# Kernel optimization log

Hardware: AMD Instinct MI355X
Metric: run time of the kernel (lower is better)

## Reference

```python
import jax, jax.numpy as jnp
import numpy as np

N = 100000
E = 3200000
F_IN = 128
HID = 128
NC = 10
G = 512  # number of graphs in batch


def setup_inputs() -> dict:
    key = jax.random.key(0)
    ks = jax.random.split(key, 9)
    x = jax.random.normal(ks[0], (N, F_IN), dtype=jnp.float32)
    edge_index = jax.random.randint(ks[1], (2, E), 0, N, dtype=jnp.int64)
    batch = jnp.sort(jax.random.randint(ks[2], (N,), 0, G, dtype=jnp.int64))
    s = 1.0 / np.sqrt(F_IN)
    W1 = jax.random.uniform(ks[3], (F_IN, HID), jnp.float32, -s, s)
    b1 = jnp.zeros((HID,), jnp.float32)
    sh = 1.0 / np.sqrt(HID)
    W2 = jax.random.uniform(ks[4], (HID, HID), jnp.float32, -sh, sh)
    b2 = jnp.zeros((HID,), jnp.float32)
    Wc = jax.random.uniform(ks[5], (HID, NC), jnp.float32, -sh, sh)
    bc = jax.random.uniform(ks[6], (NC,), jnp.float32, -sh, sh)
    return {"x": x, "edge_index": edge_index, "batch": batch,
            "W1": W1, "b1": b1, "W2": W2, "b2": b2, "Wc": Wc, "bc": bc}


def _gcn_conv(x, src, dst, norm, W, b):
    # linear transform first (PyG GCNConv), then normalized scatter-add
    h = x @ W                              # [N, H]
    msg = h[src] * norm[:, None]           # gather + scale, [E+N, H]
    out = jax.ops.segment_sum(msg, dst, num_segments=N)
    return out + b


def reference(x, edge_index, batch, W1, b1, W2, b2, Wc, bc):
    # add self-loops (PyG gcn_norm default)
    loop = jnp.arange(N, dtype=edge_index.dtype)
    src = jnp.concatenate([edge_index[0], loop])
    dst = jnp.concatenate([edge_index[1], loop])
    deg = jax.ops.segment_sum(jnp.ones_like(dst, dtype=x.dtype), dst, num_segments=N)
    dis = jnp.where(deg > 0, jax.lax.rsqrt(deg), 0.0)  # deg^{-1/2}
    norm = dis[src] * dis[dst]

    h = jax.nn.relu(_gcn_conv(x, src, dst, norm, W1, b1))
    # dropout is identity in eval mode
    h = jax.nn.relu(_gcn_conv(h, src, dst, norm, W2, b2))

    # global mean pool over graph ids
    sums = jax.ops.segment_sum(h, batch, num_segments=G)
    cnts = jax.ops.segment_sum(jnp.ones((N,), h.dtype), batch, num_segments=G)
    pooled = sums / jnp.maximum(cnts, 1.0)[:, None]   # [G, HID]

    logits = pooled @ Wc + bc                          # [G, NC]
    return logits, pooled
```

## Files before the change

kernel.cpp:

```cpp
#include <hip/hip_runtime.h>
#include <hip/hip_bf16.h>

typedef short bf16x8 __attribute__((ext_vector_type(8)));
typedef float f32x4 __attribute__((ext_vector_type(4)));
typedef unsigned int u32x4 __attribute__((ext_vector_type(4)));

__device__ __forceinline__ unsigned short f2bf(float f) {
    unsigned int u = __float_as_uint(f);
    unsigned int r = u + 0x7fffu + ((u >> 16) & 1u);
    return (unsigned short)(r >> 16);
}
__device__ __forceinline__ float bf2f(unsigned short b) {
    return __uint_as_float(((unsigned int)b) << 16);
}

__global__ __launch_bounds__(256) void cast_bf_k(const float* __restrict__ x, unsigned short* __restrict__ o, int n4) {
    int i = blockIdx.x * 256 + threadIdx.x;
    if (i < n4) {
        float4 v = ((const float4*)x)[i];
        ushort4 r;
        r.x = f2bf(v.x); r.y = f2bf(v.y); r.z = f2bf(v.z); r.w = f2bf(v.w);
        ((ushort4*)o)[i] = r;
    }
}

__global__ __launch_bounds__(256) void hist_k(const int* __restrict__ dst, int* __restrict__ hist,
                                              int e, int nbuk, int nblk, int eb) {
    __shared__ int lh[512];
    int blk = blockIdx.x, t = threadIdx.x;
    for (int j = t; j < nbuk; j += 256) lh[j] = 0;
    __syncthreads();
    int e0 = blk * eb, e1 = min(e, e0 + eb);
    for (int i = e0 + t; i < e1; i += 256) atomicAdd(&lh[dst[i] >> 8], 1);
    __syncthreads();
    for (int j = t; j < nbuk; j += 256) hist[(size_t)j * nblk + blk] = lh[j];
}

__global__ __launch_bounds__(256) void scanA_k(int* __restrict__ hist, int* __restrict__ btot, int nbuk, int nblk) {
    int w = (blockIdx.x * 256 + threadIdx.x) >> 6;
    int lane = threadIdx.x & 63;
    if (w >= nbuk) return;
    size_t base = (size_t)w * nblk;
    int run = 0;
    for (int c = 0; c < nblk; c += 64) {
        int i = c + lane;
        int v = (i < nblk) ? hist[base + i] : 0;
        int orig = v;
        for (int d = 1; d < 64; d <<= 1) { int u = __shfl_up(v, d); if (lane >= d) v += u; }
        if (i < nblk) hist[base + i] = run + v - orig;
        run += __shfl(v, 63);
    }
    if (lane == 0) btot[w] = run;
}

__global__ __launch_bounds__(512) void scanB_k(const int* __restrict__ btot, int* __restrict__ bbase, int nbuk) {
    __shared__ int s[512];
    int t = threadIdx.x;
    int v = (t < nbuk) ? btot[t] : 0;
    s[t] = v;
    __syncthreads();
    for (int st = 1; st < 512; st <<= 1) {
        int add = (t >= st) ? s[t - st] : 0;
        __syncthreads();
        s[t] += add;
        __syncthreads();
    }
    if (t < nbuk) bbase[t] = s[t] - v;
    if (t == nbuk - 1) bbase[nbuk] = s[t];
}

__global__ __launch_bounds__(256) void scatter_k(const int* __restrict__ src, const int* __restrict__ dst,
                                                 const int* __restrict__ hist, const int* __restrict__ bbase,
                                                 unsigned int* __restrict__ coarse, int e, int nbuk, int nblk, int eb) {
    __shared__ int cur[512];
    int blk = blockIdx.x, t = threadIdx.x;
    for (int j = t; j < nbuk; j += 256) cur[j] = bbase[j] + hist[(size_t)j * nblk + blk];
    __syncthreads();
    int e0 = blk * eb, e1 = min(e, e0 + eb);
    for (int i = e0 + t; i < e1; i += 256) {
        int s = src[i], d = dst[i];
        int bk = d >> 8;
        int p = atomicAdd(&cur[bk], 1);
        coarse[p] = ((unsigned int)(d & 255) << 24) | (unsigned int)s;
    }
}

__global__ __launch_bounds__(256) void bucket_k(const unsigned int* __restrict__ coarse, const int* __restrict__ bbase,
                                                int* __restrict__ cnt, int* __restrict__ row_ptr, int* __restrict__ col,
                                                int n, int nbuk, int e) {
    __shared__ int h[256];
    __shared__ int s[256];
    __shared__ int cur[256];
    int b = blockIdx.x, t = threadIdx.x;
    int e0 = bbase[b], e1 = bbase[b + 1];
    h[t] = 0;
    __syncthreads();
    for (int i = e0 + t; i < e1; i += 256) atomicAdd(&h[coarse[i] >> 24], 1);
    __syncthreads();
    int v = h[t];
    s[t] = v;
    __syncthreads();
    for (int st = 1; st < 256; st <<= 1) {
        int add = (t >= st) ? s[t - st] : 0;
        __syncthreads();
        s[t] += add;
        __syncthreads();
    }
    int excl = s[t] - v;
    int node = b * 256 + t;
    if (node < n) { cnt[node] = v; row_ptr[node] = e0 + excl; }
    cur[t] = e0 + excl;
    __syncthreads();
    for (int i = e0 + t; i < e1; i += 256) {
        unsigned int pk = coarse[i];
        int p = atomicAdd(&cur[pk >> 24], 1);
        col[p] = (int)(pk & 0x00FFFFFFu);
    }
    if (b == nbuk - 1 && t == 0) row_ptr[n] = e;
}

__global__ __launch_bounds__(256) void dis_k(const int* __restrict__ cnt, float* __restrict__ dis, int n) {
    int i = blockIdx.x * 256 + threadIdx.x;
    if (i < n) dis[i] = rsqrtf((float)cnt[i] + 1.0f);
}

__global__ __launch_bounds__(256) void gemm_mfma_k(const unsigned short* __restrict__ A, const float* __restrict__ W,
                                                   const float* __restrict__ dis, unsigned short* __restrict__ C,
                                                   int nrows) {
    __shared__ unsigned short WT[128 * 136];
    int t = threadIdx.x;
    for (int i = t; i < 16384; i += 256) {
        int k = i >> 7, nn = i & 127;
        WT[nn * 136 + k] = f2bf(W[i]);
    }
    __syncthreads();
    int wave = t >> 6, lane = t & 63;
    int lm = lane & 15, lg = lane >> 4;
    for (int m0 = blockIdx.x * 64; m0 < nrows; m0 += gridDim.x * 64) {
        int R = m0 + wave * 16;
        int arow = R + lm;
        if (arow >= nrows) arow = nrows - 1;
        const u32x4* ap = (const u32x4*)(A + (size_t)arow * 128);
        f32x4 acc[8];
#pragma unroll
        for (int q = 0; q < 8; q++) acc[q] = (f32x4){0.f, 0.f, 0.f, 0.f};
#pragma unroll
        for (int kk = 0; kk < 4; kk++) {
            bf16x8 af = __builtin_bit_cast(bf16x8, ap[kk * 4 + lg]);
#pragma unroll
            for (int q = 0; q < 8; q++) {
                const u32x4* bp = (const u32x4*)(WT + (q * 16 + lm) * 136 + kk * 32 + lg * 8);
                bf16x8 bfr = __builtin_bit_cast(bf16x8, *bp);
                acc[q] = __builtin_amdgcn_mfma_f32_16x16x32_bf16(af, bfr, acc[q], 0, 0, 0);
            }
        }
        float dsc[4];
#pragma unroll
        for (int i2 = 0; i2 < 4; i2++) {
            int r = R + lg * 4 + i2;
            dsc[i2] = (r < nrows) ? dis[r] : 0.f;
        }
#pragma unroll
        for (int i2 = 0; i2 < 4; i2++) {
            int r = R + lg * 4 + i2;
            if (r < nrows) {
                unsigned short* cp = C + (size_t)r * 128 + lm;
#pragma unroll
                for (int q = 0; q < 8; q++) cp[q * 16] = f2bf(acc[q][i2] * dsc[i2]);
            }
        }
    }
}

__global__ __launch_bounds__(256) void agg_k(const unsigned short* __restrict__ h, unsigned short* __restrict__ out,
                                             const int* __restrict__ row_ptr, const int* __restrict__ col,
                                             const float* __restrict__ dis, const float* __restrict__ bias, int n) {
    int wid  = (blockIdx.x * 256 + threadIdx.x) >> 6;
    int lane = threadIdx.x & 63;
    if (wid >= n) return;
    const unsigned int* hp = (const unsigned int*)h;
    unsigned int hv = hp[(size_t)wid * 64 + lane];
    float accx = __uint_as_float(hv << 16);
    float accy = __uint_as_float(hv & 0xffff0000u);
    int e = row_ptr[wid], e1 = row_ptr[wid + 1];
    for (; e + 8 <= e1; e += 8) {
        int c0 = col[e],     c1 = col[e + 1], c2 = col[e + 2], c3 = col[e + 3];
        int c4 = col[e + 4], c5 = col[e + 5], c6 = col[e + 6], c7 = col[e + 7];
        unsigned int h0 = hp[(size_t)c0 * 64 + lane];
        unsigned int h1 = hp[(size_t)c1 * 64 + lane];
        unsigned int h2 = hp[(size_t)c2 * 64 + lane];
        unsigned int h3 = hp[(size_t)c3 * 64 + lane];
        unsigned int h4 = hp[(size_t)c4 * 64 + lane];
        unsigned int h5 = hp[(size_t)c5 * 64 + lane];
        unsigned int h6 = hp[(size_t)c6 * 64 + lane];
        unsigned int h7 = hp[(size_t)c7 * 64 + lane];
        accx += __uint_as_float(h0 << 16) + __uint_as_float(h1 << 16)
              + __uint_as_float(h2 << 16) + __uint_as_float(h3 << 16)
              + __uint_as_float(h4 << 16) + __uint_as_float(h5 << 16)
              + __uint_as_float(h6 << 16) + __uint_as_float(h7 << 16);
        accy += __uint_as_float(h0 & 0xffff0000u) + __uint_as_float(h1 & 0xffff0000u)
              + __uint_as_float(h2 & 0xffff0000u) + __uint_as_float(h3 & 0xffff0000u)
              + __uint_as_float(h4 & 0xffff0000u) + __uint_as_float(h5 & 0xffff0000u)
              + __uint_as_float(h6 & 0xffff0000u) + __uint_as_float(h7 & 0xffff0000u);
    }
    for (; e < e1; e++) {
        unsigned int hh = hp[(size_t)col[e] * 64 + lane];
        accx += __uint_as_float(hh << 16);
        accy += __uint_as_float(hh & 0xffff0000u);
    }
    float d = dis[wid];
    float2 b = ((const float2*)bias)[lane];
    unsigned int res = ((unsigned int)f2bf(fmaxf(b.y + d * accy, 0.f)) << 16)
                     |  (unsigned int)f2bf(fmaxf(b.x + d * accx, 0.f));
    ((unsigned int*)out)[(size_t)wid * 64 + lane] = res;
}

__global__ __launch_bounds__(128) void pool_k(const unsigned short* __restrict__ h, const int* __restrict__ batch,
                                              float* __restrict__ pooled, int n) {
    int g = blockIdx.x;
    int j = threadIdx.x;
    int lo = 0, hi = n;
    while (lo < hi) { int mid = (lo + hi) >> 1; if (batch[mid] < g) lo = mid + 1; else hi = mid; }
    int start = lo;
    hi = n;
    while (lo < hi) { int mid = (lo + hi) >> 1; if (batch[mid] < g + 1) lo = mid + 1; else hi = mid; }
    int end = lo;
    float acc = 0.f;
    for (int r = start; r < end; r++) acc += bf2f(h[(size_t)r * 128 + j]);
    float cntf = (float)(end - start);
    pooled[(size_t)g * 128 + j] = acc / fmaxf(cntf, 1.0f);
}

__global__ __launch_bounds__(64) void logits_k(const float* __restrict__ pooled, const float* __restrict__ Wc,
                                               const float* __restrict__ bc, float* __restrict__ out, int nc) {
    int g = blockIdx.x;
    int j = threadIdx.x;
    if (j >= nc) return;
    float acc = bc[j];
    const float* p = pooled + (size_t)g * 128;
#pragma unroll 8
    for (int k = 0; k < 128; k++) acc += p[k] * Wc[k * nc + j];
    out[(size_t)g * nc + j] = acc;
}

extern "C" void kernel_launch(void* const* d_in, const int* in_sizes, int n_in,
                              void* d_out, int out_size, void* d_ws, size_t ws_size,
                              hipStream_t stream) {
    const float* x     = (const float*)d_in[0];
    const int*   ei    = (const int*)d_in[1];
    const int*   batch = (const int*)d_in[2];
    const float* W1    = (const float*)d_in[3];
    const float* b1    = (const float*)d_in[4];
    const float* W2    = (const float*)d_in[5];
    const float* b2    = (const float*)d_in[6];
    const float* Wc    = (const float*)d_in[7];
    const float* bc    = (const float*)d_in[8];
    float* out = (float*)d_out;

    const int N = in_sizes[0] / 128;
    const int E = in_sizes[1] / 2;
    const int NC = 10;
    const int G = out_size / (NC + 128);

    const int* src = ei;
    const int* dst = ei + E;

    const int EB   = 16384;
    const int NBLK = (E + EB - 1) / EB;
    const int NBUK = (N + 255) / 256;

    char* wbase = (char*)d_ws;
    size_t off = 0;
    auto alloc = [&](size_t bytes) -> void* {
        void* p = wbase + off;
        off = (off + bytes + 255) & ~(size_t)255;
        return p;
    };
    int*   cnt     = (int*)alloc((size_t)N * 4);
    float* dis     = (float*)alloc((size_t)N * 4);
    int*   row_ptr = (int*)alloc((size_t)(N + 1) * 4);
    int*   hist    = (int*)alloc((size_t)NBUK * NBLK * 4);
    int*   btot    = (int*)alloc((size_t)NBUK * 4);
    int*   bbase   = (int*)alloc((size_t)(NBUK + 1) * 4);
    unsigned int* coarse = (unsigned int*)alloc((size_t)E * 4);
    int*   col     = (int*)alloc((size_t)E * 4);
    unsigned short* bufX = (unsigned short*)alloc((size_t)N * 128 * 2);
    unsigned short* bufT = (unsigned short*)alloc((size_t)N * 128 * 2);
    unsigned short* bufH = (unsigned short*)alloc((size_t)N * 128 * 2);

    hist_k<<<NBLK, 256, 0, stream>>>(dst, hist, E, NBUK, NBLK, EB);
    scanA_k<<<(NBUK * 64 + 255) / 256, 256, 0, stream>>>(hist, btot, NBUK, NBLK);
    scanB_k<<<1, 512, 0, stream>>>(btot, bbase, NBUK);
    scatter_k<<<NBLK, 256, 0, stream>>>(src, dst, hist, bbase, coarse, E, NBUK, NBLK, EB);
    bucket_k<<<NBUK, 256, 0, stream>>>(coarse, bbase, cnt, row_ptr, col, N, NBUK, E);
    dis_k<<<(N + 255) / 256, 256, 0, stream>>>(cnt, dis, N);

    cast_bf_k<<<(N * 128 / 4 + 255) / 256, 256, 0, stream>>>(x, bufX, N * 128 / 4);

    gemm_mfma_k<<<512, 256, 0, stream>>>(bufX, W1, dis, bufT, N);
    agg_k<<<(N + 3) / 4, 256, 0, stream>>>(bufT, bufH, row_ptr, col, dis, b1, N);
    gemm_mfma_k<<<512, 256, 0, stream>>>(bufH, W2, dis, bufT, N);
    agg_k<<<(N + 3) / 4, 256, 0, stream>>>(bufT, bufH, row_ptr, col, dis, b2, N);

    float* pooled = out + (size_t)G * NC;
    pool_k<<<G, 128, 0, stream>>>(bufH, batch, pooled, N);
    logits_k<<<G, 64, 0, stream>>>(pooled, Wc, bc, out, NC);
}
```

Measured before the change: 431.8 us.

## Vectorize aggregation gathers with 16-byte loads and fuse small kernels

The aggregation kernel now splits each wavefront into four groups of 16 lanes. Each lane loads 16 bytes per neighbor row, and each group handles every fourth edge. Partial sums are combined with cross-lane shuffles before the bias, ReLU and bf16 store. Separately, the degree-normalization kernel is folded into bucket_k, and pooling and logits are fused into one kernel, which removes launches and an intermediate count buffer. The wider loads should cut the number of memory instructions per gathered row and raise bytes in flight, at the cost of extra shuffle reductions and idle lanes on low-degree nodes.

```diff
diff --git a/kernel.cpp b/kernel.cpp
--- a/kernel.cpp
+++ b/kernel.cpp
@@ -12,6 +12,9 @@
 }
 __device__ __forceinline__ float bf2f(unsigned short b) {
     return __uint_as_float(((unsigned int)b) << 16);
+}
+__device__ __forceinline__ unsigned int packbf2(float lo, float hi) {
+    return ((unsigned int)f2bf(hi) << 16) | (unsigned int)f2bf(lo);
 }
 
 __global__ __launch_bounds__(256) void cast_bf_k(const float* __restrict__ x, unsigned short* __restrict__ o, int n4) {
@@ -86,7 +89,7 @@
 }
 
 __global__ __launch_bounds__(256) void bucket_k(const unsigned int* __restrict__ coarse, const int* __restrict__ bbase,
-                                                int* __restrict__ cnt, int* __restrict__ row_ptr, int* __restrict__ col,
+                                                float* __restrict__ dis, int* __restrict__ row_ptr, int* __restrict__ col,
                                                 int n, int nbuk, int e) {
     __shared__ int h[256];
     __shared__ int s[256];
@@ -108,7 +111,10 @@
     }
     int excl = s[t] - v;
     int node = b * 256 + t;
-    if (node < n) { cnt[node] = v; row_ptr[node] = e0 + excl; }
+    if (node < n) {
+        row_ptr[node] = e0 + excl;
+        dis[node] = rsqrtf((float)v + 1.0f);
+    }
     cur[t] = e0 + excl;
     __syncthreads();
     for (int i = e0 + t; i < e1; i += 256) {
@@ -117,11 +123,6 @@
         col[p] = (int)(pk & 0x00FFFFFFu);
     }
     if (b == nbuk - 1 && t == 0) row_ptr[n] = e;
-}
-
-__global__ __launch_bounds__(256) void dis_k(const int* __restrict__ cnt, float* __restrict__ dis, int n) {
-    int i = blockIdx.x * 256 + threadIdx.x;
-    if (i < n) dis[i] = rsqrtf((float)cnt[i] + 1.0f);
 }
 
 __global__ __launch_bounds__(256) void gemm_mfma_k(const unsigned short* __restrict__ A, const float* __restrict__ W,
@@ -178,45 +179,56 @@
     int wid  = (blockIdx.x * 256 + threadIdx.x) >> 6;
     int lane = threadIdx.x & 63;
     if (wid >= n) return;
-    const unsigned int* hp = (const unsigned int*)h;
-    unsigned int hv = hp[(size_t)wid * 64 + lane];
-    float accx = __uint_as_float(hv << 16);
-    float accy = __uint_as_float(hv & 0xffff0000u);
-    int e = row_ptr[wid], e1 = row_ptr[wid + 1];
-    for (; e + 8 <= e1; e += 8) {
-        int c0 = col[e],     c1 = col[e + 1], c2 = col[e + 2], c3 = col[e + 3];
-        int c4 = col[e + 4], c5 = col[e + 5], c6 = col[e + 6], c7 = col[e + 7];
-        unsigned int h0 = hp[(size_t)c0 * 64 + lane];
-        unsigned int h1 = hp[(size_t)c1 * 64 + lane];
-        unsigned int h2 = hp[(size_t)c2 * 64 + lane];
-        unsigned int h3 = hp[(size_t)c3 * 64 + lane];
-        unsigned int h4 = hp[(size_t)c4 * 64 + lane];
-        unsigned int h5 = hp[(size_t)c5 * 64 + lane];
-        unsigned int h6 = hp[(size_t)c6 * 64 + lane];
-        unsigned int h7 = hp[(size_t)c7 * 64 + lane];
-        accx += __uint_as_float(h0 << 16) + __uint_as_float(h1 << 16)
-              + __uint_as_float(h2 << 16) + __uint_as_float(h3 << 16)
-              + __uint_as_float(h4 << 16) + __uint_as_float(h5 << 16)
-              + __uint_as_float(h6 << 16) + __uint_as_float(h7 << 16);
-        accy += __uint_as_float(h0 & 0xffff0000u) + __uint_as_float(h1 & 0xffff0000u)
-              + __uint_as_float(h2 & 0xffff0000u) + __uint_as_float(h3 & 0xffff0000u)
-              + __uint_as_float(h4 & 0xffff0000u) + __uint_as_float(h5 & 0xffff0000u)
-              + __uint_as_float(h6 & 0xffff0000u) + __uint_as_float(h7 & 0xffff0000u);
-    }
-    for (; e < e1; e++) {
-        unsigned int hh = hp[(size_t)col[e] * 64 + lane];
-        accx += __uint_as_float(hh << 16);
-        accy += __uint_as_float(hh & 0xffff0000u);
-    }
-    float d = dis[wid];
-    float2 b = ((const float2*)bias)[lane];
-    unsigned int res = ((unsigned int)f2bf(fmaxf(b.y + d * accy, 0.f)) << 16)
-                     |  (unsigned int)f2bf(fmaxf(b.x + d * accx, 0.f));
-    ((unsigned int*)out)[(size_t)wid * 64 + lane] = res;
-}
-
-__global__ __launch_bounds__(128) void pool_k(const unsigned short* __restrict__ h, const int* __restrict__ batch,
-                                              float* __restrict__ pooled, int n) {
+    int g = lane >> 4;
+    int s = lane & 15;
+    const char* hb = (const char*)h;
+    unsigned int soff = (unsigned int)(s << 4);
+    float acc0 = 0.f, acc1 = 0.f, acc2 = 0.f, acc3 = 0.f;
+    float acc4 = 0.f, acc5 = 0.f, acc6 = 0.f, acc7 = 0.f;
+#define ACCUM(v)                                                                              \
+    acc0 += __uint_as_float((v)[0] << 16); acc1 += __uint_as_float((v)[0] & 0xffff0000u);     \
+    acc2 += __uint_as_float((v)[1] << 16); acc3 += __uint_as_float((v)[1] & 0xffff0000u);     \
+    acc4 += __uint_as_float((v)[2] << 16); acc5 += __uint_as_float((v)[2] & 0xffff0000u);     \
+    acc6 += __uint_as_float((v)[3] << 16); acc7 += __uint_as_float((v)[3] & 0xffff0000u);
+    if (g == 0) {
+        u32x4 v = *(const u32x4*)(hb + (((unsigned int)wid << 8) + soff));
+        ACCUM(v)
+    }
+    int e = row_ptr[wid] + g, e1 = row_ptr[wid + 1];
+    for (; e + 4 < e1; e += 8) {
+        unsigned int o0 = ((unsigned int)col[e] << 8) + soff;
+        unsigned int o1 = ((unsigned int)col[e + 4] << 8) + soff;
+        u32x4 v0 = *(const u32x4*)(hb + o0);
+        u32x4 v1 = *(const u32x4*)(hb + o1);
+        ACCUM(v0)
+        ACCUM(v1)
+    }
+    if (e < e1) {
+        u32x4 v0 = *(const u32x4*)(hb + (((unsigned int)col[e] << 8) + soff));
+        ACCUM(v0)
+    }
+#undef ACCUM
+#define RED(a) a += __shfl_xor(a, 16); a += __shfl_xor(a, 32);
+    RED(acc0) RED(acc1) RED(acc2) RED(acc3) RED(acc4) RED(acc5) RED(acc6) RED(acc7)
+#undef RED
+    if (g == 0) {
+        float d = dis[wid];
+        const float4* bp = (const float4*)bias;
+        float4 ba = bp[2 * s], bb = bp[2 * s + 1];
+        u32x4 r;
+        r[0] = packbf2(fmaxf(ba.x + d * acc0, 0.f), fmaxf(ba.y + d * acc1, 0.f));
+        r[1] = packbf2(fmaxf(ba.z + d * acc2, 0.f), fmaxf(ba.w + d * acc3, 0.f));
+        r[2] = packbf2(fmaxf(bb.x + d * acc4, 0.f), fmaxf(bb.y + d * acc5, 0.f));
+        r[3] = packbf2(fmaxf(bb.z + d * acc6, 0.f), fmaxf(bb.w + d * acc7, 0.f));
+        *(u32x4*)((char*)out + (((unsigned int)wid << 8) + soff)) = r;
+    }
+}
+
+__global__ __launch_bounds__(128) void pool_logits_k(const unsigned short* __restrict__ h, const int* __restrict__ batch,
+                                                     const float* __restrict__ Wc, const float* __restrict__ bc,
+                                                     float* __restrict__ logits, float* __restrict__ pooled,
+                                                     int n, int nc) {
+    __shared__ float pl[128];
     int g = blockIdx.x;
     int j = threadIdx.x;
     int lo = 0, hi = n;
@@ -227,20 +239,16 @@
     int end = lo;
     float acc = 0.f;
     for (int r = start; r < end; r++) acc += bf2f(h[(size_t)r * 128 + j]);
-    float cntf = (float)(end - start);
-    pooled[(size_t)g * 128 + j] = acc / fmaxf(cntf, 1.0f);
-}
-
-__global__ __launch_bounds__(64) void logits_k(const float* __restrict__ pooled, const float* __restrict__ Wc,
-                                               const float* __restrict__ bc, float* __restrict__ out, int nc) {
-    int g = blockIdx.x;
-    int j = threadIdx.x;
-    if (j >= nc) return;
-    float acc = bc[j];
-    const float* p = pooled + (size_t)g * 128;
+    float pv = acc / fmaxf((float)(end - start), 1.0f);
+    pooled[(size_t)g * 128 + j] = pv;
+    pl[j] = pv;
+    __syncthreads();
+    if (j < nc) {
+        float a = bc[j];
 #pragma unroll 8
-    for (int k = 0; k < 128; k++) acc += p[k] * Wc[k * nc + j];
-    out[(size_t)g * nc + j] = acc;
+        for (int k = 0; k < 128; k++) a += pl[k] * Wc[k * nc + j];
+        logits[(size_t)g * nc + j] = a;
+    }
 }
 
 extern "C" void kernel_launch(void* const* d_in, const int* in_sizes, int n_in,
@@ -276,7 +284,6 @@
         off = (off + bytes + 255) & ~(size_t)255;
         return p;
     };
-    int*   cnt     = (int*)alloc((size_t)N * 4);
     float* dis     = (float*)alloc((size_t)N * 4);
     int*   row_ptr = (int*)alloc((size_t)(N + 1) * 4);
     int*   hist    = (int*)alloc((size_t)NBUK * NBLK * 4);
@@ -292,8 +299,7 @@
     scanA_k<<<(NBUK * 64 + 255) / 256, 256, 0, stream>>>(hist, btot, NBUK, NBLK);
     scanB_k<<<1, 512, 0, stream>>>(btot, bbase, NBUK);
     scatter_k<<<NBLK, 256, 0, stream>>>(src, dst, hist, bbase, coarse, E, NBUK, NBLK, EB);
-    bucket_k<<<NBUK, 256, 0, stream>>>(coarse, bbase, cnt, row_ptr, col, N, NBUK, E);
-    dis_k<<<(N + 255) / 256, 256, 0, stream>>>(cnt, dis, N);
+    bucket_k<<<NBUK, 256, 0, stream>>>(coarse, bbase, dis, row_ptr, col, N, NBUK, E);
 
     cast_bf_k<<<(N * 128 / 4 + 255) / 256, 256, 0, stream>>>(x, bufX, N * 128 / 4);
 
@@ -303,6 +309,5 @@
     agg_k<<<(N + 3) / 4, 256, 0, stream>>>(bufT, bufH, row_ptr, col, dis, b2, N);
 
     float* pooled = out + (size_t)G * NC;
-    pool_k<<<G, 128, 0, stream>>>(bufH, batch, pooled, N);
-    logits_k<<<G, 64, 0, stream>>>(pooled, Wc, bc, out, NC);
-}
+    pool_logits_k<<<G, 128, 0, stream>>>(bufH, batch, Wc, bc, out, pooled, N, NC);
+}
```

Result: faster. 415.6 us (-3.7%).
